# Performance work log

Hardware: AMD Instinct MI355X
Metric: run time of the kernel (lower is better)

The kernel has to match this reference:

```python
import jax, jax.numpy as jnp
import numpy as np

B, L1, L2 = 16, 32, 128
DEC = 512       # decoder_size
MEM = 512       # memory_bank_size
TOP = 50        # topic_num


def setup_inputs() -> dict:
    key = jax.random.key(0)
    ks = jax.random.split(key, 16)
    s = lambda fan_in: 1.0 / np.sqrt(fan_in)
    inp = {
        "decoder_state": jax.random.normal(ks[0], (B, DEC), jnp.float32),
        "doc_memory": jax.random.normal(ks[1], (B, L1, MEM), jnp.float32),
        "word_memory": jax.random.normal(ks[2], (B, L1, L2, MEM), jnp.float32),
        "topic_dist": jax.random.uniform(ks[3], (B, TOP), jnp.float32),
        "doc_mask": jnp.ones((B, L1), jnp.int32),
        "word_mask": jnp.ones((B, L1, L2), jnp.int32),
        # HierAttention params (PyTorch Linear weight layout: [out, in])
        "Wv": jax.random.uniform(ks[4], (1, DEC), jnp.float32, -s(DEC), s(DEC)),
        "Wd": jax.random.uniform(ks[5], (DEC, DEC), jnp.float32, -s(DEC), s(DEC)),
        "Wt": jax.random.uniform(ks[6], (DEC, TOP), jnp.float32, -s(TOP), s(TOP)),
        "Wm": jax.random.uniform(ks[7], (DEC, MEM), jnp.float32, -s(MEM), s(MEM)),
        # doc_attention (inner Attention) params
        "Wv2": jax.random.uniform(ks[8], (1, DEC), jnp.float32, -s(DEC), s(DEC)),
        "Wd2": jax.random.uniform(ks[9], (DEC, DEC), jnp.float32, -s(DEC), s(DEC)),
        "Wt2": jax.random.uniform(ks[10], (DEC, TOP), jnp.float32, -s(TOP), s(TOP)),
        "Wm2": jax.random.uniform(ks[11], (DEC, MEM), jnp.float32, -s(MEM), s(MEM)),
    }
    return inp


def reference(decoder_state, doc_memory, word_memory, topic_dist,
              doc_mask, word_mask,
              Wv, Wd, Wt, Wm, Wv2, Wd2, Wt2, Wm2):
    neg_inf = jnp.float32(-jnp.inf)

    # ---- word-level (HierAttention.score) ----
    enc_feat = jnp.einsum('bqwm,dm->bqwd', word_memory, Wm)      # [B,L1,L2,DEC]
    dec_feat = decoder_state @ Wd.T                              # [B,DEC]
    top_feat = topic_dist @ Wt.T                                 # [B,DEC]
    e = jnp.tanh(enc_feat + (dec_feat + top_feat)[:, None, None, :])
    word_scores = jnp.einsum('bqwd,od->bqw', e, Wv)[..., 0] if Wv.shape[0] != 1 else jnp.einsum('bqwd,d->bqw', e, Wv[0])
    word_scores = jnp.where(word_mask == 0, neg_inf, word_scores)
    word_attn = jax.nn.softmax(word_scores, axis=-1)             # [B,L1,L2]

    # ---- doc-level (Attention.score) ----
    enc_feat_d = jnp.einsum('bqm,dm->bqd', doc_memory, Wm2)      # [B,L1,DEC]
    dec_feat_d = decoder_state @ Wd2.T                           # [B,DEC]
    top_feat_d = topic_dist @ Wt2.T                              # [B,DEC]
    e_d = jnp.tanh(enc_feat_d + (dec_feat_d + top_feat_d)[:, None, :])
    doc_scores = jnp.einsum('bqd,d->bq', e_d, Wv2[0])            # [B,L1]
    doc_scores = jnp.where(doc_mask == 0, neg_inf, doc_scores)
    doc_attn = jax.nn.softmax(doc_scores, axis=-1)               # [B,L1]

    # ---- combine ----
    rescaled = doc_attn[..., None] * word_attn                   # [B,L1,L2]
    context = jnp.einsum('bqw,bqwm->bm', rescaled, word_memory)  # [B,MEM]
    return context, rescaled
```

## Files before the change

kernel.cpp:

```cpp
#include <hip/hip_runtime.h>
#include <hip/hip_bf16.h>
#include <math.h>

#define BATCH 16
#define L1 32
#define L2 128
#define DEC 512
#define MEM 512
#define TOPN 50
#define NROWS (BATCH * L1 * L2)
#define NBQ (BATCH * L1)

typedef short short8 __attribute__((ext_vector_type(8)));
typedef float f32x16 __attribute__((ext_vector_type(16)));

#define WS_WP     0
#define WS_WP2    131072
#define WS_BIAS1  262144
#define WS_BIAS2  270336
#define WS_DOCSC  278528

__device__ __forceinline__ unsigned int pkbf(float a, float b) {
    __hip_bfloat162 h = __float22bfloat162_rn(float2{a, b});
    union { __hip_bfloat162 h; unsigned int u; } c{h};
    return c.u;
}

__device__ __forceinline__ float fast_tanh(float x) {
    return 1.f - 2.f / (__expf(2.f * x) + 1.f);
}

__global__ __launch_bounds__(256) void setup_kernel(
    const float* __restrict__ Wm, const float* __restrict__ Wm2,
    unsigned short* __restrict__ Wp, unsigned short* __restrict__ Wp2,
    const float* __restrict__ dec, const float* __restrict__ topic,
    const float* __restrict__ Wd, const float* __restrict__ Wt,
    const float* __restrict__ Wd2, const float* __restrict__ Wt2,
    float* __restrict__ bias1, float* __restrict__ bias2,
    float* __restrict__ ctx_out)
{
    if (blockIdx.x < 128) {
        int s = blockIdx.x * 256 + threadIdx.x;
        int C = s >> 10;
        int u = s & 1023;
        int nt = u >> 6, k8 = (u >> 5) & 1, n_in = u & 31;
        int d = nt * 32 + n_in;
        int k = C * 16 + k8 * 8;

        const float* src = Wm + (size_t)d * DEC + k;
        uint4 v;
        v.x = pkbf(src[0], src[1]); v.y = pkbf(src[2], src[3]);
        v.z = pkbf(src[4], src[5]); v.w = pkbf(src[6], src[7]);
        ((uint4*)Wp)[s] = v;

        const float* src2 = Wm2 + (size_t)d * DEC + k;
        uint4 w;
        w.x = pkbf(src2[0], src2[1]); w.y = pkbf(src2[2], src2[3]);
        w.z = pkbf(src2[4], src2[5]); w.w = pkbf(src2[6], src2[7]);
        ((uint4*)Wp2)[s] = w;
    } else if (blockIdx.x < 160) {
        int idx = (blockIdx.x - 128) * 256 + threadIdx.x;
        int b = idx >> 9, d = idx & 511;
        float a1 = 0.f, a2 = 0.f;
        const float* db = dec + b * DEC;
        const float* w1 = Wd + (size_t)d * DEC;
        const float* w2 = Wd2 + (size_t)d * DEC;
#pragma unroll 4
        for (int k = 0; k < DEC; ++k) {
            float x = db[k];
            a1 = fmaf(x, w1[k], a1);
            a2 = fmaf(x, w2[k], a2);
        }
        const float* tb = topic + b * TOPN;
        const float* t1 = Wt + (size_t)d * TOPN;
        const float* t2 = Wt2 + (size_t)d * TOPN;
#pragma unroll 2
        for (int t = 0; t < TOPN; ++t) {
            float x = tb[t];
            a1 = fmaf(x, t1[t], a1);
            a2 = fmaf(x, t2[t], a2);
        }
        bias1[idx] = a1;
        bias2[idx] = a2;
    } else {
        int i = (blockIdx.x - 160) * 256 + threadIdx.x;
        float4 z = {0.f, 0.f, 0.f, 0.f};
        ((float4*)ctx_out)[i * 2] = z;
        ((float4*)ctx_out)[i * 2 + 1] = z;
    }
}

__global__ __launch_bounds__(256) void score_mfma_kernel(
    const float* __restrict__ X,
    const unsigned short* __restrict__ Wp,
    const float* __restrict__ Wv,
    const float* __restrict__ bias,
    float* __restrict__ scores,
    int bshift)
{
    __shared__ __align__(16) short lsA[256 * 8];
    __shared__ __align__(16) short lsB[2048 * 8];
    __shared__ float red[4][64];

    const int tid = threadIdx.x;
    const int lane = tid & 63;
    const int wid = tid >> 6;
    const int row0 = blockIdx.x * 64;

    const int srow = tid >> 2;
    const int kslot = tid & 3;
    const int sA = ((kslot >> 1) * 2 + (srow >> 5)) * 64 + (kslot & 1) * 32 + (srow & 31);
    const float4* xs4 = (const float4*)(X + (size_t)(row0 + srow) * DEC) + kslot * 2;

    const uint4* bsrc = (const uint4*)Wp + (size_t)wid * 512 + lane;

    f32x16 acc[8];
#pragma unroll
    for (int t = 0; t < 8; ++t)
        acc[t] = (f32x16){0.f,0.f,0.f,0.f, 0.f,0.f,0.f,0.f, 0.f,0.f,0.f,0.f, 0.f,0.f,0.f,0.f};

    const short8* lA = (const short8*)lsA;
    const short8* lB = (const short8*)lsB;

    for (int it = 0; it < 16; ++it) {
        uint4 bv[8];
#pragma unroll
        for (int i = 0; i < 8; ++i) bv[i] = bsrc[i * 64];
        bsrc += 2048;
#pragma unroll
        for (int i = 0; i < 8; ++i)
            *((uint4*)&lsB[((size_t)wid * 512 + i * 64 + lane) * 8]) = bv[i];

        float4 xv0 = xs4[0];
        float4 xv1 = xs4[1];
        xs4 += 8;
        union { unsigned int u[4]; short8 s; } xb;
        xb.u[0] = pkbf(xv0.x, xv0.y); xb.u[1] = pkbf(xv0.z, xv0.w);
        xb.u[2] = pkbf(xv1.x, xv1.y); xb.u[3] = pkbf(xv1.z, xv1.w);
        *((short8*)&lsA[sA * 8]) = xb.s;

        __syncthreads();

#pragma unroll
        for (int c = 0; c < 2; ++c) {
            short8 a0 = lA[(c * 2 + 0) * 64 + lane];
            short8 a1 = lA[(c * 2 + 1) * 64 + lane];
            short8 b0 = lB[c * 1024 + (wid * 4 + 0) * 64 + lane];
            short8 b1 = lB[c * 1024 + (wid * 4 + 1) * 64 + lane];
            short8 b2 = lB[c * 1024 + (wid * 4 + 2) * 64 + lane];
            short8 b3 = lB[c * 1024 + (wid * 4 + 3) * 64 + lane];
            acc[0] = __builtin_amdgcn_mfma_f32_32x32x16_bf16(a0, b0, acc[0], 0, 0, 0);
            acc[1] = __builtin_amdgcn_mfma_f32_32x32x16_bf16(a0, b1, acc[1], 0, 0, 0);
            acc[2] = __builtin_amdgcn_mfma_f32_32x32x16_bf16(a0, b2, acc[2], 0, 0, 0);
            acc[3] = __builtin_amdgcn_mfma_f32_32x32x16_bf16(a0, b3, acc[3], 0, 0, 0);
            acc[4] = __builtin_amdgcn_mfma_f32_32x32x16_bf16(a1, b0, acc[4], 0, 0, 0);
            acc[5] = __builtin_amdgcn_mfma_f32_32x32x16_bf16(a1, b1, acc[5], 0, 0, 0);
            acc[6] = __builtin_amdgcn_mfma_f32_32x32x16_bf16(a1, b2, acc[6], 0, 0, 0);
            acc[7] = __builtin_amdgcn_mfma_f32_32x32x16_bf16(a1, b3, acc[7], 0, 0, 0);
        }
        __syncthreads();
    }

    const int col = lane & 31;
    const int h = lane >> 5;
    float wv[4], bs[2][4];
    const int b0i = (row0) >> bshift;
    const int b1i = (row0 + 32) >> bshift;
#pragma unroll
    for (int nt = 0; nt < 4; ++nt) {
        int d = wid * 128 + nt * 32 + col;
        wv[nt] = Wv[d];
        bs[0][nt] = bias[b0i * DEC + d];
        bs[1][nt] = bias[b1i * DEC + d];
    }

#pragma unroll
    for (int mt = 0; mt < 2; ++mt) {
#pragma unroll
        for (int r = 0; r < 16; ++r) {
            float p = 0.f;
#pragma unroll
            for (int nt = 0; nt < 4; ++nt) {
                float x = acc[mt * 4 + nt][r] + bs[mt][nt];
                p = fmaf(wv[nt], fast_tanh(x), p);
            }
            p += __shfl_xor(p, 16);
            p += __shfl_xor(p, 8);
            p += __shfl_xor(p, 4);
            p += __shfl_xor(p, 2);
            p += __shfl_xor(p, 1);
            if (col == mt * 16 + r) {
                int row_in = (r & 3) + 8 * (r >> 2) + 4 * h;
                red[wid][mt * 32 + row_in] = p;
            }
        }
    }
    __syncthreads();
    if (tid < 64)
        scores[row0 + tid] = red[0][tid] + red[1][tid] + red[2][tid] + red[3][tid];
}

__global__ __launch_bounds__(512) void fused_word_kernel(
    const float* __restrict__ X,
    const unsigned short* __restrict__ Wp,
    const float* __restrict__ Wv,
    const float* __restrict__ bias1,
    const float* __restrict__ doc_scores,
    const int* __restrict__ doc_mask,
    const int* __restrict__ word_mask,
    float* __restrict__ rescaled_out,
    float* __restrict__ ctx_out)
{
    __shared__ __align__(16) short lsA[2 * 2048];
    __shared__ float red[8][128];
    __shared__ float sS[128];
    __shared__ float rmax2[2], rsum2[2];
    __shared__ float s_dattn;
    __shared__ __align__(16) float4 part[3 * 128];

    const int tid = threadIdx.x;
    const int lane = tid & 63;
    const int wid = tid >> 6;
    const int bq = blockIdx.x;
    const int r0 = bq * L2;
    const int b = bq >> 5;
    const int q = bq & 31;

    if (tid < 32) {
        int di = b * 32 + tid;
        float dsv = doc_scores[di];
        if (doc_mask[di] == 0) dsv = -INFINITY;
        float mx = dsv;
#pragma unroll
        for (int o = 1; o <= 16; o <<= 1) mx = fmaxf(mx, __shfl_xor(mx, o));
        float e = __expf(dsv - mx);
        float sum = e;
#pragma unroll
        for (int o = 1; o <= 16; o <<= 1) sum += __shfl_xor(sum, o);
        if (tid == q) s_dattn = e / sum;
    }

    const int row = tid >> 2;
    const int kq = tid & 3;
    const int mt_s = row >> 5;
    const int rl_s = row & 31;
    const int k8_s = kq >> 1;
    const int q4 = (kq & 1) * 4;
    const int slot_s = mt_s * 64 + k8_s * 32 + rl_s;
    const float4* xs = (const float4*)(X + (size_t)(r0 + row) * DEC) + kq;

    const uint4* Bp = (const uint4*)Wp;
    const int boff = wid * 128 + lane;

    f32x16 acc[8];
#pragma unroll
    for (int t = 0; t < 8; ++t)
        acc[t] = (f32x16){0.f,0.f,0.f,0.f, 0.f,0.f,0.f,0.f, 0.f,0.f,0.f,0.f, 0.f,0.f,0.f,0.f};

    const short8* lA = (const short8*)lsA;

    float4 va[4];
#pragma unroll
    for (int i = 0; i < 4; ++i) va[i] = xs[i * 4];
    uint4 ub0[2], ub1[2];
#pragma unroll
    for (int i = 0; i < 2; ++i) {
        ub0[i] = Bp[i * 1024 + boff];
        ub1[i] = Bp[i * 1024 + boff + 64];
    }

#pragma unroll
    for (int c = 0; c < 32; ++c) {
        const int p = c & 1;
        const int ia = c & 3;
        uint2 w2;
        w2.x = pkbf(va[ia].x, va[ia].y);
        w2.y = pkbf(va[ia].z, va[ia].w);
        *(uint2*)&lsA[(p * 256 + slot_s) * 8 + q4] = w2;
        __syncthreads();

        va[ia] = xs[((c + 4) & 31) * 4];
        uint4 nb0 = Bp[((c + 2) & 31) * 1024 + boff];
        uint4 nb1 = Bp[((c + 2) & 31) * 1024 + boff + 64];

        short8 a0 = lA[p * 256 + 0 * 64 + lane];
        short8 a1 = lA[p * 256 + 1 * 64 + lane];
        short8 a2 = lA[p * 256 + 2 * 64 + lane];
        short8 a3 = lA[p * 256 + 3 * 64 + lane];
        union { uint4 u; short8 s; } cb0{ub0[p]}, cb1{ub1[p]};
        acc[0] = __builtin_amdgcn_mfma_f32_32x32x16_bf16(a0, cb0.s, acc[0], 0, 0, 0);
        acc[1] = __builtin_amdgcn_mfma_f32_32x32x16_bf16(a0, cb1.s, acc[1], 0, 0, 0);
        acc[2] = __builtin_amdgcn_mfma_f32_32x32x16_bf16(a1, cb0.s, acc[2], 0, 0, 0);
        acc[3] = __builtin_amdgcn_mfma_f32_32x32x16_bf16(a1, cb1.s, acc[3], 0, 0, 0);
        acc[4] = __builtin_amdgcn_mfma_f32_32x32x16_bf16(a2, cb0.s, acc[4], 0, 0, 0);
        acc[5] = __builtin_amdgcn_mfma_f32_32x32x16_bf16(a2, cb1.s, acc[5], 0, 0, 0);
        acc[6] = __builtin_amdgcn_mfma_f32_32x32x16_bf16(a3, cb0.s, acc[6], 0, 0, 0);
        acc[7] = __builtin_amdgcn_mfma_f32_32x32x16_bf16(a3, cb1.s, acc[7], 0, 0, 0);

        ub0[p] = nb0; ub1[p] = nb1;
    }

    const int col = lane & 31;
    const int h = lane >> 5;
    float wv0, wv1, bs0, bs1;
    {
        int d0 = wid * 64 + col;
        int d1 = wid * 64 + 32 + col;
        wv0 = Wv[d0]; wv1 = Wv[d1];
        bs0 = bias1[b * DEC + d0]; bs1 = bias1[b * DEC + d1];
    }
#pragma unroll
    for (int mt = 0; mt < 4; ++mt) {
#pragma unroll
        for (int r = 0; r < 16; ++r) {
            float p = fmaf(wv0, fast_tanh(acc[mt * 2 + 0][r] + bs0),
                           wv1 * fast_tanh(acc[mt * 2 + 1][r] + bs1));
            p += __shfl_xor(p, 16);
            p += __shfl_xor(p, 8);
            p += __shfl_xor(p, 4);
            p += __shfl_xor(p, 2);
            p += __shfl_xor(p, 1);
            if (col == r) {
                int row_in = (r & 3) + 8 * (r >> 2) + 4 * h;
                red[wid][mt * 32 + row_in] = p;
            }
        }
    }
    __syncthreads();

    float e = 0.f, sv = 0.f;
    if (tid < 128) {
        sv = red[0][tid] + red[1][tid] + red[2][tid] + red[3][tid]
           + red[4][tid] + red[5][tid] + red[6][tid] + red[7][tid];
        if (word_mask[r0 + tid] == 0) sv = -INFINITY;
        float mx = sv;
#pragma unroll
        for (int o = 1; o <= 32; o <<= 1) mx = fmaxf(mx, __shfl_xor(mx, o));
        if (lane == 0) rmax2[wid] = mx;
    }
    __syncthreads();
    if (tid < 128) {
        float mx = fmaxf(rmax2[0], rmax2[1]);
        e = __expf(sv - mx);
        float sum = e;
#pragma unroll
        for (int o = 1; o <= 32; o <<= 1) sum += __shfl_xor(sum, o);
        if (lane == 0) rsum2[wid] = sum;
    }
    __syncthreads();
    if (tid < 128) {
        float sum = rsum2[0] + rsum2[1];
        float resc = s_dattn * (e / sum);
        sS[tid] = resc;
        rescaled_out[r0 + tid] = resc;
    }
    __syncthreads();

    const int hh = tid >> 7;
    const int m4 = tid & 127;
    const float4* Xr = (const float4*)X + (size_t)r0 * 128 + (size_t)hh * 32 * 128 + m4;
    float4 a = {0.f, 0.f, 0.f, 0.f};
#pragma unroll 8
    for (int i = 0; i < 32; ++i) {
        float rr = sS[hh * 32 + i];
        float4 v = Xr[(size_t)i * 128];
        a.x = fmaf(rr, v.x, a.x);
        a.y = fmaf(rr, v.y, a.y);
        a.z = fmaf(rr, v.z, a.z);
        a.w = fmaf(rr, v.w, a.w);
    }
    if (hh) part[(hh - 1) * 128 + m4] = a;
    __syncthreads();
    if (hh == 0) {
        float4 p0 = part[m4], p1 = part[128 + m4], p2 = part[256 + m4];
        a.x += p0.x + p1.x + p2.x;
        a.y += p0.y + p1.y + p2.y;
        a.z += p0.z + p1.z + p2.z;
        a.w += p0.w + p1.w + p2.w;
        float* dst = ctx_out + (size_t)b * MEM + m4 * 4;
        atomicAdd(dst + 0, a.x);
        atomicAdd(dst + 1, a.y);
        atomicAdd(dst + 2, a.z);
        atomicAdd(dst + 3, a.w);
    }
}

extern "C" void kernel_launch(void* const* d_in, const int* in_sizes, int n_in,
                              void* d_out, int out_size, void* d_ws, size_t ws_size,
                              hipStream_t stream) {
    const float* decoder_state = (const float*)d_in[0];
    const float* doc_memory    = (const float*)d_in[1];
    const float* word_memory   = (const float*)d_in[2];
    const float* topic_dist    = (const float*)d_in[3];
    const int*   doc_mask      = (const int*)d_in[4];
    const int*   word_mask     = (const int*)d_in[5];
    const float* Wv  = (const float*)d_in[6];
    const float* Wd  = (const float*)d_in[7];
    const float* Wt  = (const float*)d_in[8];
    const float* Wm  = (const float*)d_in[9];
    const float* Wv2 = (const float*)d_in[10];
    const float* Wd2 = (const float*)d_in[11];
    const float* Wt2 = (const float*)d_in[12];
    const float* Wm2 = (const float*)d_in[13];

    float* ws = (float*)d_ws;
    unsigned short* Wp  = (unsigned short*)(ws + WS_WP);
    unsigned short* Wp2 = (unsigned short*)(ws + WS_WP2);
    float* bias1       = ws + WS_BIAS1;
    float* bias2       = ws + WS_BIAS2;
    float* doc_scores  = ws + WS_DOCSC;

    float* ctx_out      = (float*)d_out;
    float* rescaled_out = (float*)d_out + BATCH * MEM;

    setup_kernel<<<164, 256, 0, stream>>>(Wm, Wm2, Wp, Wp2,
                                          decoder_state, topic_dist,
                                          Wd, Wt, Wd2, Wt2, bias1, bias2, ctx_out);
    score_mfma_kernel<<<NBQ / 64, 256, 0, stream>>>(doc_memory, Wp2, Wv2, bias2, doc_scores, 5);
    fused_word_kernel<<<NBQ, 512, 0, stream>>>(word_memory, Wp, Wv, bias1,
                                               doc_scores, doc_mask, word_mask,
                                               rescaled_out, ctx_out);
}
```

Baseline: 350.3 us.

## Process two K-chunks per barrier with four LDS buffers and MFMA priority

Restructures the main GEMM loop of the fused word kernel so that each iteration stages two K-chunks of the activation tile into a four-slot LDS ring. Only one barrier is issued per pair of chunks, which halves the number of workgroup barriers. The barrier is now a raw s_barrier preceded by an explicit lgkmcnt wait. The MFMA sequences are wrapped in s_setprio to favour matrix issue across waves. This raises LDS usage and register pressure from the extra weight prefetch buffers, which could lower occupancy.

```diff
diff --git a/kernel.cpp b/kernel.cpp
--- a/kernel.cpp
+++ b/kernel.cpp
@@ -211,7 +211,7 @@
     float* __restrict__ rescaled_out,
     float* __restrict__ ctx_out)
 {
-    __shared__ __align__(16) short lsA[2 * 2048];
+    __shared__ __align__(16) short lsA[4 * 2048];
     __shared__ float red[8][128];
     __shared__ float sS[128];
     __shared__ float rmax2[2], rsum2[2];
@@ -262,42 +262,73 @@
     float4 va[4];
 #pragma unroll
     for (int i = 0; i < 4; ++i) va[i] = xs[i * 4];
-    uint4 ub0[2], ub1[2];
-#pragma unroll
-    for (int i = 0; i < 2; ++i) {
-        ub0[i] = Bp[i * 1024 + boff];
-        ub1[i] = Bp[i * 1024 + boff + 64];
-    }
-
-#pragma unroll
-    for (int c = 0; c < 32; ++c) {
-        const int p = c & 1;
-        const int ia = c & 3;
-        uint2 w2;
-        w2.x = pkbf(va[ia].x, va[ia].y);
-        w2.y = pkbf(va[ia].z, va[ia].w);
-        *(uint2*)&lsA[(p * 256 + slot_s) * 8 + q4] = w2;
-        __syncthreads();
-
-        va[ia] = xs[((c + 4) & 31) * 4];
-        uint4 nb0 = Bp[((c + 2) & 31) * 1024 + boff];
-        uint4 nb1 = Bp[((c + 2) & 31) * 1024 + boff + 64];
-
-        short8 a0 = lA[p * 256 + 0 * 64 + lane];
-        short8 a1 = lA[p * 256 + 1 * 64 + lane];
-        short8 a2 = lA[p * 256 + 2 * 64 + lane];
-        short8 a3 = lA[p * 256 + 3 * 64 + lane];
-        union { uint4 u; short8 s; } cb0{ub0[p]}, cb1{ub1[p]};
-        acc[0] = __builtin_amdgcn_mfma_f32_32x32x16_bf16(a0, cb0.s, acc[0], 0, 0, 0);
-        acc[1] = __builtin_amdgcn_mfma_f32_32x32x16_bf16(a0, cb1.s, acc[1], 0, 0, 0);
-        acc[2] = __builtin_amdgcn_mfma_f32_32x32x16_bf16(a1, cb0.s, acc[2], 0, 0, 0);
-        acc[3] = __builtin_amdgcn_mfma_f32_32x32x16_bf16(a1, cb1.s, acc[3], 0, 0, 0);
-        acc[4] = __builtin_amdgcn_mfma_f32_32x32x16_bf16(a2, cb0.s, acc[4], 0, 0, 0);
-        acc[5] = __builtin_amdgcn_mfma_f32_32x32x16_bf16(a2, cb1.s, acc[5], 0, 0, 0);
-        acc[6] = __builtin_amdgcn_mfma_f32_32x32x16_bf16(a3, cb0.s, acc[6], 0, 0, 0);
-        acc[7] = __builtin_amdgcn_mfma_f32_32x32x16_bf16(a3, cb1.s, acc[7], 0, 0, 0);
-
-        ub0[p] = nb0; ub1[p] = nb1;
+    uint4 ubb[2][2][2];
+#pragma unroll
+    for (int j = 0; j < 2; ++j) {
+        ubb[0][j][0] = Bp[j * 1024 + boff];
+        ubb[0][j][1] = Bp[j * 1024 + boff + 64];
+    }
+
+#pragma unroll
+    for (int cc = 0; cc < 16; ++cc) {
+        const int c0 = cc * 2, c1 = cc * 2 + 1;
+        const int b0 = c0 & 3, b1 = c1 & 3;
+        const int s = cc & 1;
+
+        {
+            uint2 w0, w1;
+            w0.x = pkbf(va[b0].x, va[b0].y);
+            w0.y = pkbf(va[b0].z, va[b0].w);
+            w1.x = pkbf(va[b1].x, va[b1].y);
+            w1.y = pkbf(va[b1].z, va[b1].w);
+            *(uint2*)&lsA[(b0 * 256 + slot_s) * 8 + q4] = w0;
+            *(uint2*)&lsA[(b1 * 256 + slot_s) * 8 + q4] = w1;
+        }
+        asm volatile("s_waitcnt lgkmcnt(0)" ::: "memory");
+        __builtin_amdgcn_s_barrier();
+        asm volatile("" ::: "memory");
+
+        va[b0] = xs[((c0 + 4) & 31) * 4];
+        va[b1] = xs[((c1 + 4) & 31) * 4];
+        ubb[s ^ 1][0][0] = Bp[((c0 + 2) & 31) * 1024 + boff];
+        ubb[s ^ 1][0][1] = Bp[((c0 + 2) & 31) * 1024 + boff + 64];
+        ubb[s ^ 1][1][0] = Bp[((c1 + 2) & 31) * 1024 + boff];
+        ubb[s ^ 1][1][1] = Bp[((c1 + 2) & 31) * 1024 + boff + 64];
+
+        {
+            short8 a0 = lA[b0 * 256 + 0 * 64 + lane];
+            short8 a1 = lA[b0 * 256 + 1 * 64 + lane];
+            short8 a2 = lA[b0 * 256 + 2 * 64 + lane];
+            short8 a3 = lA[b0 * 256 + 3 * 64 + lane];
+            union { uint4 u; short8 s8; } cb0{ubb[s][0][0]}, cb1{ubb[s][0][1]};
+            __builtin_amdgcn_s_setprio(1);
+            acc[0] = __builtin_amdgcn_mfma_f32_32x32x16_bf16(a0, cb0.s8, acc[0], 0, 0, 0);
+            acc[1] = __builtin_amdgcn_mfma_f32_32x32x16_bf16(a0, cb1.s8, acc[1], 0, 0, 0);
+            acc[2] = __builtin_amdgcn_mfma_f32_32x32x16_bf16(a1, cb0.s8, acc[2], 0, 0, 0);
+            acc[3] = __builtin_amdgcn_mfma_f32_32x32x16_bf16(a1, cb1.s8, acc[3], 0, 0, 0);
+            acc[4] = __builtin_amdgcn_mfma_f32_32x32x16_bf16(a2, cb0.s8, acc[4], 0, 0, 0);
+            acc[5] = __builtin_amdgcn_mfma_f32_32x32x16_bf16(a2, cb1.s8, acc[5], 0, 0, 0);
+            acc[6] = __builtin_amdgcn_mfma_f32_32x32x16_bf16(a3, cb0.s8, acc[6], 0, 0, 0);
+            acc[7] = __builtin_amdgcn_mfma_f32_32x32x16_bf16(a3, cb1.s8, acc[7], 0, 0, 0);
+            __builtin_amdgcn_s_setprio(0);
+        }
+        {
+            short8 a0 = lA[b1 * 256 + 0 * 64 + lane];
+            short8 a1 = lA[b1 * 256 + 1 * 64 + lane];
+            short8 a2 = lA[b1 * 256 + 2 * 64 + lane];
+            short8 a3 = lA[b1 * 256 + 3 * 64 + lane];
+            union { uint4 u; short8 s8; } cb0{ubb[s][1][0]}, cb1{ubb[s][1][1]};
+            __builtin_amdgcn_s_setprio(1);
+            acc[0] = __builtin_amdgcn_mfma_f32_32x32x16_bf16(a0, cb0.s8, acc[0], 0, 0, 0);
+            acc[1] = __builtin_amdgcn_mfma_f32_32x32x16_bf16(a0, cb1.s8, acc[1], 0, 0, 0);
+            acc[2] = __builtin_amdgcn_mfma_f32_32x32x16_bf16(a1, cb0.s8, acc[2], 0, 0, 0);
+            acc[3] = __builtin_amdgcn_mfma_f32_32x32x16_bf16(a1, cb1.s8, acc[3], 0, 0, 0);
+            acc[4] = __builtin_amdgcn_mfma_f32_32x32x16_bf16(a2, cb0.s8, acc[4], 0, 0, 0);
+            acc[5] = __builtin_amdgcn_mfma_f32_32x32x16_bf16(a2, cb1.s8, acc[5], 0, 0, 0);
+            acc[6] = __builtin_amdgcn_mfma_f32_32x32x16_bf16(a3, cb0.s8, acc[6], 0, 0, 0);
+            acc[7] = __builtin_amdgcn_mfma_f32_32x32x16_bf16(a3, cb1.s8, acc[7], 0, 0, 0);
+            __builtin_amdgcn_s_setprio(0);
+        }
     }
 
     const int col = lane & 31;
```

New measurement: 352.4 us. Within noise of the previous version (+0.6%).

## Stage full bf16 A tile in LDS once and split N into two passes

Applied to the files above, without the earlier changes.

The fused word kernel used to convert X to bf16 in small double-buffered LDS chunks with a barrier on every k-step. It now converts the whole 128x512 A tile into a padded LDS buffer using four barriers. The 8 waves are split 2 (rows) x 4 (columns), and the 512 output columns are covered in two passes of 256 with 4 accumulators each, running the tanh/Wv epilogue after each pass. The goal is to cut per-step barriers and accumulator register pressure, at the cost of about 132KB of LDS per block, which limits occupancy to one block per CU.

```diff
diff --git a/kernel.cpp b/kernel.cpp
--- a/kernel.cpp
+++ b/kernel.cpp
@@ -211,7 +211,7 @@
     float* __restrict__ rescaled_out,
     float* __restrict__ ctx_out)
 {
-    __shared__ __align__(16) short lsA[2 * 2048];
+    __shared__ __align__(16) char lsA[64 * 2064];
     __shared__ float red[8][128];
     __shared__ float sS[128];
     __shared__ float rmax2[2], rsum2[2];
@@ -221,10 +221,74 @@
     const int tid = threadIdx.x;
     const int lane = tid & 63;
     const int wid = tid >> 6;
+    const int wr = wid & 1;
+    const int wd = wid >> 1;
     const int bq = blockIdx.x;
     const int r0 = bq * L2;
     const int b = bq >> 5;
     const int q = bq & 31;
+    const int col = lane & 31;
+    const int h = lane >> 5;
+
+    const float4* Xs = (const float4*)X + (size_t)(r0 + (tid >> 5)) * 128 + (tid & 31);
+    char* const wbase = lsA + (((tid & 31) >> 1) * 2064) + ((tid >> 5) << 4) + ((tid & 1) << 3);
+
+#define ISSUE(dst, ks) { _Pragma("unroll") \
+    for (int i = 0; i < 8; ++i) dst[i] = Xs[(size_t)(i * 16) * 128 + (ks) * 32]; }
+
+#define WRITEA(src, ks) { char* wp = wbase + (ks) * 16 * 2064; _Pragma("unroll") \
+    for (int i = 0; i < 8; ++i) { uint2 w; \
+        w.x = pkbf(src[i].x, src[i].y); w.y = pkbf(src[i].z, src[i].w); \
+        *(uint2*)(wp + i * 256) = w; } }
+
+#define LGKMBAR { asm volatile("s_waitcnt lgkmcnt(0)" ::: "memory"); \
+                  __builtin_amdgcn_s_barrier(); asm volatile("" ::: "memory"); }
+
+    const uint4* Bp = (const uint4*)Wp;
+    const size_t bB = (size_t)wd * 128 + lane;
+#define BOFFC(t, nt) ((size_t)(((t) & 31)) * 1024 + ((((t) >> 5) & 1)) * 512 + bB + (nt) * 64)
+
+    const char* const aP = lsA + (lane >> 5) * 2064 + ((wr * 64) + (lane & 31)) * 16;
+#define MFMA(a, bb, c) __builtin_amdgcn_mfma_f32_32x32x16_bf16(a, bb, c, 0, 0, 0)
+
+    f32x16 acc[4];
+#pragma unroll
+    for (int t = 0; t < 4; ++t)
+        acc[t] = (f32x16){0.f,0.f,0.f,0.f, 0.f,0.f,0.f,0.f, 0.f,0.f,0.f,0.f, 0.f,0.f,0.f,0.f};
+
+    uint4 ub[2][2];
+
+#define CHUNK(t) { \
+    union { uint4 u; short8 s8; } c0{ub[(t) & 1][0]}, c1{ub[(t) & 1][1]}; \
+    ub[(t) & 1][0] = Bp[BOFFC(((t) + 2) & 63, 0)]; \
+    ub[(t) & 1][1] = Bp[BOFFC(((t) + 2) & 63, 1)]; \
+    short8 a0 = *(const short8*)(aP + ((t) & 31) * 4128); \
+    short8 a1 = *(const short8*)(aP + ((t) & 31) * 4128 + 512); \
+    acc[0] = MFMA(a0, c0.s8, acc[0]); \
+    acc[1] = MFMA(a0, c1.s8, acc[1]); \
+    acc[2] = MFMA(a1, c0.s8, acc[2]); \
+    acc[3] = MFMA(a1, c1.s8, acc[3]); }
+
+#define CHUNK8(base) { CHUNK((base)+0) CHUNK((base)+1) CHUNK((base)+2) CHUNK((base)+3) \
+                       CHUNK((base)+4) CHUNK((base)+5) CHUNK((base)+6) CHUNK((base)+7) }
+
+#define EPILOGUE(p) { \
+    int d0 = (p) * 256 + wd * 64 + col; \
+    float wv0 = Wv[d0], wv1 = Wv[d0 + 32]; \
+    float bs0 = bias1[b * DEC + d0], bs1 = bias1[b * DEC + d0 + 32]; \
+    _Pragma("unroll") for (int mt = 0; mt < 2; ++mt) { \
+      _Pragma("unroll") for (int r = 0; r < 16; ++r) { \
+        float val = fmaf(wv0, fast_tanh(acc[mt * 2 + 0][r] + bs0), \
+                         wv1 * fast_tanh(acc[mt * 2 + 1][r] + bs1)); \
+        val += __shfl_xor(val, 16); val += __shfl_xor(val, 8); \
+        val += __shfl_xor(val, 4);  val += __shfl_xor(val, 2); \
+        val += __shfl_xor(val, 1); \
+        if (col == r) red[(p) * 4 + wd][wr * 64 + mt * 32 + ((r & 3) + 8 * (r >> 2) + 4 * h)] = val; \
+      } } }
+
+    float4 vA[8], vB[8];
+    ISSUE(vA, 0);
+    ISSUE(vB, 1);
 
     if (tid < 32) {
         int di = b * 32 + tid;
@@ -240,92 +304,64 @@
         if (tid == q) s_dattn = e / sum;
     }
 
-    const int row = tid >> 2;
-    const int kq = tid & 3;
-    const int mt_s = row >> 5;
-    const int rl_s = row & 31;
-    const int k8_s = kq >> 1;
-    const int q4 = (kq & 1) * 4;
-    const int slot_s = mt_s * 64 + k8_s * 32 + rl_s;
-    const float4* xs = (const float4*)(X + (size_t)(r0 + row) * DEC) + kq;
-
-    const uint4* Bp = (const uint4*)Wp;
-    const int boff = wid * 128 + lane;
-
-    f32x16 acc[8];
-#pragma unroll
-    for (int t = 0; t < 8; ++t)
+    WRITEA(vA, 0);
+    ub[0][0] = Bp[BOFFC(0, 0)];
+    ub[0][1] = Bp[BOFFC(0, 1)];
+    ub[1][0] = Bp[BOFFC(1, 0)];
+    ub[1][1] = Bp[BOFFC(1, 1)];
+    LGKMBAR;
+    ISSUE(vA, 2);
+    CHUNK8(0);
+    WRITEA(vB, 1);
+    LGKMBAR;
+    ISSUE(vB, 3);
+    CHUNK8(8);
+    WRITEA(vA, 2);
+    LGKMBAR;
+    CHUNK8(16);
+    WRITEA(vB, 3);
+    LGKMBAR;
+    CHUNK8(24);
+
+    EPILOGUE(0);
+
+#pragma unroll
+    for (int t = 0; t < 4; ++t)
         acc[t] = (f32x16){0.f,0.f,0.f,0.f, 0.f,0.f,0.f,0.f, 0.f,0.f,0.f,0.f, 0.f,0.f,0.f,0.f};
 
-    const short8* lA = (const short8*)lsA;
-
-    float4 va[4];
-#pragma unroll
-    for (int i = 0; i < 4; ++i) va[i] = xs[i * 4];
-    uint4 ub0[2], ub1[2];
-#pragma unroll
-    for (int i = 0; i < 2; ++i) {
-        ub0[i] = Bp[i * 1024 + boff];
-        ub1[i] = Bp[i * 1024 + boff + 64];
-    }
-
-#pragma unroll
-    for (int c = 0; c < 32; ++c) {
-        const int p = c & 1;
-        const int ia = c & 3;
-        uint2 w2;
-        w2.x = pkbf(va[ia].x, va[ia].y);
-        w2.y = pkbf(va[ia].z, va[ia].w);
-        *(uint2*)&lsA[(p * 256 + slot_s) * 8 + q4] = w2;
-        __syncthreads();
-
-        va[ia] = xs[((c + 4) & 31) * 4];
-        uint4 nb0 = Bp[((c + 2) & 31) * 1024 + boff];
-        uint4 nb1 = Bp[((c + 2) & 31) * 1024 + boff + 64];
-
-        short8 a0 = lA[p * 256 + 0 * 64 + lane];
-        short8 a1 = lA[p * 256 + 1 * 64 + lane];
-        short8 a2 = lA[p * 256 + 2 * 64 + lane];
-        short8 a3 = lA[p * 256 + 3 * 64 + lane];
-        union { uint4 u; short8 s; } cb0{ub0[p]}, cb1{ub1[p]};
-        acc[0] = __builtin_amdgcn_mfma_f32_32x32x16_bf16(a0, cb0.s, acc[0], 0, 0, 0);
-        acc[1] = __builtin_amdgcn_mfma_f32_32x32x16_bf16(a0, cb1.s, acc[1], 0, 0, 0);
-        acc[2] = __builtin_amdgcn_mfma_f32_32x32x16_bf16(a1, cb0.s, acc[2], 0, 0, 0);
-        acc[3] = __builtin_amdgcn_mfma_f32_32x32x16_bf16(a1, cb1.s, acc[3], 0, 0, 0);
-        acc[4] = __builtin_amdgcn_mfma_f32_32x32x16_bf16(a2, cb0.s, acc[4], 0, 0, 0);
-        acc[5] = __builtin_amdgcn_mfma_f32_32x32x16_bf16(a2, cb1.s, acc[5], 0, 0, 0);
-        acc[6] = __builtin_amdgcn_mfma_f32_32x32x16_bf16(a3, cb0.s, acc[6], 0, 0, 0);
-        acc[7] = __builtin_amdgcn_mfma_f32_32x32x16_bf16(a3, cb1.s, acc[7], 0, 0, 0);
-
-        ub0[p] = nb0; ub1[p] = nb1;
-    }
-
-    const int col = lane & 31;
-    const int h = lane >> 5;
-    float wv0, wv1, bs0, bs1;
-    {
-        int d0 = wid * 64 + col;
-        int d1 = wid * 64 + 32 + col;
-        wv0 = Wv[d0]; wv1 = Wv[d1];
-        bs0 = bias1[b * DEC + d0]; bs1 = bias1[b * DEC + d1];
-    }
-#pragma unroll
-    for (int mt = 0; mt < 4; ++mt) {
-#pragma unroll
-        for (int r = 0; r < 16; ++r) {
-            float p = fmaf(wv0, fast_tanh(acc[mt * 2 + 0][r] + bs0),
-                           wv1 * fast_tanh(acc[mt * 2 + 1][r] + bs1));
-            p += __shfl_xor(p, 16);
-            p += __shfl_xor(p, 8);
-            p += __shfl_xor(p, 4);
-            p += __shfl_xor(p, 2);
-            p += __shfl_xor(p, 1);
-            if (col == r) {
-                int row_in = (r & 3) + 8 * (r >> 2) + 4 * h;
-                red[wid][mt * 32 + row_in] = p;
-            }
-        }
-    }
+#pragma unroll 2
+    for (int j = 0; j < 16; ++j) {
+        const int c0 = 2 * j, c1 = 2 * j + 1;
+        {
+            union { uint4 u; short8 s8; } d00{ub[0][0]}, d01{ub[0][1]};
+            int tt = (32 + c0 + 2) & 63;
+            size_t off = (size_t)(tt & 31) * 1024 + ((tt >> 5) & 1) * 512 + bB;
+            ub[0][0] = Bp[off];
+            ub[0][1] = Bp[off + 64];
+            short8 a0 = *(const short8*)(aP + c0 * 4128);
+            short8 a1 = *(const short8*)(aP + c0 * 4128 + 512);
+            acc[0] = MFMA(a0, d00.s8, acc[0]);
+            acc[1] = MFMA(a0, d01.s8, acc[1]);
+            acc[2] = MFMA(a1, d00.s8, acc[2]);
+            acc[3] = MFMA(a1, d01.s8, acc[3]);
+        }
+        {
+            union { uint4 u; short8 s8; } d10{ub[1][0]}, d11{ub[1][1]};
+            int tt = (32 + c1 + 2) & 63;
+            size_t off = (size_t)(tt & 31) * 1024 + ((tt >> 5) & 1) * 512 + bB;
+            ub[1][0] = Bp[off];
+            ub[1][1] = Bp[off + 64];
+            short8 a0 = *(const short8*)(aP + c1 * 4128);
+            short8 a1 = *(const short8*)(aP + c1 * 4128 + 512);
+            acc[0] = MFMA(a0, d10.s8, acc[0]);
+            acc[1] = MFMA(a0, d11.s8, acc[1]);
+            acc[2] = MFMA(a1, d10.s8, acc[2]);
+            acc[3] = MFMA(a1, d11.s8, acc[3]);
+        }
+    }
+
+    EPILOGUE(1);
+
     __syncthreads();
 
     float e = 0.f, sv = 0.f;
```

After: 367.4 us. +4.9%, slower.

## Split word scoring from combine, merge doc/word score GEMMs, warp-parallel bias GEMV

Applied to the files above, without the earlier changes.

Pulls the word-score MFMA GEMM out of the fused per-(b,q) kernel into one score kernel that also handles the doc scores. That kernel stages a full 64x512 bf16 A tile in padded LDS once and streams B fragments from global memory through registers. A separate combine kernel then reads the raw scores back from the rescaled output buffer, applies softmax and accumulates the context. The bias GEMVs are rewritten to give one wave per output element, with vectorized loads and a shuffle reduction, replacing the serial per-thread loop. The cost is that word_memory is now read twice from global memory, and raw scores make an extra round trip through the output buffer.

```diff
diff --git a/kernel.cpp b/kernel.cpp
--- a/kernel.cpp
+++ b/kernel.cpp
@@ -39,184 +39,210 @@
     float* __restrict__ bias1, float* __restrict__ bias2,
     float* __restrict__ ctx_out)
 {
-    if (blockIdx.x < 128) {
-        int s = blockIdx.x * 256 + threadIdx.x;
+    const int bid = blockIdx.x;
+    const int tid = threadIdx.x;
+    if (bid < 128) {
+        int s = bid * 256 + tid;
         int C = s >> 10;
         int u = s & 1023;
         int nt = u >> 6, k8 = (u >> 5) & 1, n_in = u & 31;
         int d = nt * 32 + n_in;
         int k = C * 16 + k8 * 8;
 
-        const float* src = Wm + (size_t)d * DEC + k;
+        const float4* src = (const float4*)(Wm + (size_t)d * DEC + k);
+        float4 v0 = src[0], v1 = src[1];
         uint4 v;
-        v.x = pkbf(src[0], src[1]); v.y = pkbf(src[2], src[3]);
-        v.z = pkbf(src[4], src[5]); v.w = pkbf(src[6], src[7]);
+        v.x = pkbf(v0.x, v0.y); v.y = pkbf(v0.z, v0.w);
+        v.z = pkbf(v1.x, v1.y); v.w = pkbf(v1.z, v1.w);
         ((uint4*)Wp)[s] = v;
 
-        const float* src2 = Wm2 + (size_t)d * DEC + k;
+        const float4* src2 = (const float4*)(Wm2 + (size_t)d * DEC + k);
+        float4 w0 = src2[0], w1 = src2[1];
         uint4 w;
-        w.x = pkbf(src2[0], src2[1]); w.y = pkbf(src2[2], src2[3]);
-        w.z = pkbf(src2[4], src2[5]); w.w = pkbf(src2[6], src2[7]);
+        w.x = pkbf(w0.x, w0.y); w.y = pkbf(w0.z, w0.w);
+        w.z = pkbf(w1.x, w1.y); w.w = pkbf(w1.z, w1.w);
         ((uint4*)Wp2)[s] = w;
-    } else if (blockIdx.x < 160) {
-        int idx = (blockIdx.x - 128) * 256 + threadIdx.x;
-        int b = idx >> 9, d = idx & 511;
-        float a1 = 0.f, a2 = 0.f;
-        const float* db = dec + b * DEC;
-        const float* w1 = Wd + (size_t)d * DEC;
-        const float* w2 = Wd2 + (size_t)d * DEC;
-#pragma unroll 4
-        for (int k = 0; k < DEC; ++k) {
-            float x = db[k];
-            a1 = fmaf(x, w1[k], a1);
-            a2 = fmaf(x, w2[k], a2);
-        }
-        const float* tb = topic + b * TOPN;
-        const float* t1 = Wt + (size_t)d * TOPN;
-        const float* t2 = Wt2 + (size_t)d * TOPN;
-#pragma unroll 2
-        for (int t = 0; t < TOPN; ++t) {
-            float x = tb[t];
-            a1 = fmaf(x, t1[t], a1);
-            a2 = fmaf(x, t2[t], a2);
-        }
-        bias1[idx] = a1;
-        bias2[idx] = a2;
+    } else if (bid < 128 + 4096) {
+        int gw = (bid - 128) * 4 + (tid >> 6);
+        int lane = tid & 63;
+        int mat = gw >> 13;
+        int rem = gw & 8191;
+        int bb = rem >> 9;
+        int d = rem & 511;
+
+        const float* wrow = (mat ? Wd2 : Wd) + (size_t)d * DEC;
+        const float* drow = dec + (size_t)bb * DEC;
+        float4 a0 = ((const float4*)wrow)[lane * 2];
+        float4 a1 = ((const float4*)wrow)[lane * 2 + 1];
+        float4 x0 = ((const float4*)drow)[lane * 2];
+        float4 x1 = ((const float4*)drow)[lane * 2 + 1];
+        float acc = a0.x * x0.x;
+        acc = fmaf(a0.y, x0.y, acc);
+        acc = fmaf(a0.z, x0.z, acc);
+        acc = fmaf(a0.w, x0.w, acc);
+        acc = fmaf(a1.x, x1.x, acc);
+        acc = fmaf(a1.y, x1.y, acc);
+        acc = fmaf(a1.z, x1.z, acc);
+        acc = fmaf(a1.w, x1.w, acc);
+        const float* trow = (mat ? Wt2 : Wt) + (size_t)d * TOPN;
+        if (lane < TOPN) acc = fmaf(trow[lane], topic[bb * TOPN + lane], acc);
+#pragma unroll
+        for (int o = 1; o <= 32; o <<= 1) acc += __shfl_xor(acc, o);
+        if (lane == 0) (mat ? bias2 : bias1)[bb * DEC + d] = acc;
     } else {
-        int i = (blockIdx.x - 160) * 256 + threadIdx.x;
+        int i = (bid - (128 + 4096)) * 256 + tid;
         float4 z = {0.f, 0.f, 0.f, 0.f};
         ((float4*)ctx_out)[i * 2] = z;
         ((float4*)ctx_out)[i * 2 + 1] = z;
     }
 }
 
-__global__ __launch_bounds__(256) void score_mfma_kernel(
-    const float* __restrict__ X,
+__global__ __launch_bounds__(256, 2) void score_all_kernel(
+    const float* __restrict__ Xw,
+    const float* __restrict__ Xd,
     const unsigned short* __restrict__ Wp,
-    const float* __restrict__ Wv,
-    const float* __restrict__ bias,
-    float* __restrict__ scores,
-    int bshift)
+    const unsigned short* __restrict__ Wp2,
+    const float* __restrict__ Wv, const float* __restrict__ Wv2,
+    const float* __restrict__ bias1, const float* __restrict__ bias2,
+    float* __restrict__ word_scores,
+    float* __restrict__ doc_scores)
 {
-    __shared__ __align__(16) short lsA[256 * 8];
-    __shared__ __align__(16) short lsB[2048 * 8];
+    __shared__ __align__(16) char lsA[64 * 1040];
     __shared__ float red[4][64];
 
+    const int bid = blockIdx.x;
     const int tid = threadIdx.x;
+    const bool isdoc = (bid >= 1024);
+
+    const float* X;
+    const unsigned short* Wpp;
+    const float* Wvp;
+    const float* bias;
+    float* outp;
+    int r0, bshift;
+    if (isdoc) { X = Xd; Wpp = Wp2; Wvp = Wv2; bias = bias2; outp = doc_scores; r0 = (bid - 1024) * 64; bshift = 5; }
+    else       { X = Xw; Wpp = Wp;  Wvp = Wv;  bias = bias1; outp = word_scores; r0 = bid * 64; bshift = 12; }
+
+    {
+        const int kf4 = tid & 127;
+        const int rb0 = tid >> 7;
+        const float4* Xs = (const float4*)X + (size_t)r0 * 128 + kf4;
+        float4 va[8], vb[8];
+#pragma unroll
+        for (int i = 0; i < 8; ++i) va[i] = Xs[(size_t)(2 * i + rb0) * 128];
+#pragma unroll
+        for (int blk = 0; blk < 4; ++blk) {
+            float4* cur = (blk & 1) ? vb : va;
+            float4* nxt = (blk & 1) ? va : vb;
+            if (blk < 3) {
+#pragma unroll
+                for (int i = 0; i < 8; ++i)
+                    nxt[i] = Xs[(size_t)(2 * (8 * (blk + 1) + i) + rb0) * 128];
+            }
+#pragma unroll
+            for (int i = 0; i < 8; ++i) {
+                int row = 2 * (8 * blk + i) + rb0;
+                uint2 w;
+                w.x = pkbf(cur[i].x, cur[i].y);
+                w.y = pkbf(cur[i].z, cur[i].w);
+                *(uint2*)(lsA + (size_t)row * 1040 + kf4 * 8) = w;
+            }
+        }
+    }
+    __syncthreads();
+
     const int lane = tid & 63;
     const int wid = tid >> 6;
-    const int row0 = blockIdx.x * 64;
-
-    const int srow = tid >> 2;
-    const int kslot = tid & 3;
-    const int sA = ((kslot >> 1) * 2 + (srow >> 5)) * 64 + (kslot & 1) * 32 + (srow & 31);
-    const float4* xs4 = (const float4*)(X + (size_t)(row0 + srow) * DEC) + kslot * 2;
-
-    const uint4* bsrc = (const uint4*)Wp + (size_t)wid * 512 + lane;
-
-    f32x16 acc[8];
-#pragma unroll
-    for (int t = 0; t < 8; ++t)
-        acc[t] = (f32x16){0.f,0.f,0.f,0.f, 0.f,0.f,0.f,0.f, 0.f,0.f,0.f,0.f, 0.f,0.f,0.f,0.f};
-
-    const short8* lA = (const short8*)lsA;
-    const short8* lB = (const short8*)lsB;
-
-    for (int it = 0; it < 16; ++it) {
-        uint4 bv[8];
-#pragma unroll
-        for (int i = 0; i < 8; ++i) bv[i] = bsrc[i * 64];
-        bsrc += 2048;
-#pragma unroll
-        for (int i = 0; i < 8; ++i)
-            *((uint4*)&lsB[((size_t)wid * 512 + i * 64 + lane) * 8]) = bv[i];
-
-        float4 xv0 = xs4[0];
-        float4 xv1 = xs4[1];
-        xs4 += 8;
-        union { unsigned int u[4]; short8 s; } xb;
-        xb.u[0] = pkbf(xv0.x, xv0.y); xb.u[1] = pkbf(xv0.z, xv0.w);
-        xb.u[2] = pkbf(xv1.x, xv1.y); xb.u[3] = pkbf(xv1.z, xv1.w);
-        *((short8*)&lsA[sA * 8]) = xb.s;
-
-        __syncthreads();
-
-#pragma unroll
-        for (int c = 0; c < 2; ++c) {
-            short8 a0 = lA[(c * 2 + 0) * 64 + lane];
-            short8 a1 = lA[(c * 2 + 1) * 64 + lane];
-            short8 b0 = lB[c * 1024 + (wid * 4 + 0) * 64 + lane];
-            short8 b1 = lB[c * 1024 + (wid * 4 + 1) * 64 + lane];
-            short8 b2 = lB[c * 1024 + (wid * 4 + 2) * 64 + lane];
-            short8 b3 = lB[c * 1024 + (wid * 4 + 3) * 64 + lane];
-            acc[0] = __builtin_amdgcn_mfma_f32_32x32x16_bf16(a0, b0, acc[0], 0, 0, 0);
-            acc[1] = __builtin_amdgcn_mfma_f32_32x32x16_bf16(a0, b1, acc[1], 0, 0, 0);
-            acc[2] = __builtin_amdgcn_mfma_f32_32x32x16_bf16(a0, b2, acc[2], 0, 0, 0);
-            acc[3] = __builtin_amdgcn_mfma_f32_32x32x16_bf16(a0, b3, acc[3], 0, 0, 0);
-            acc[4] = __builtin_amdgcn_mfma_f32_32x32x16_bf16(a1, b0, acc[4], 0, 0, 0);
-            acc[5] = __builtin_amdgcn_mfma_f32_32x32x16_bf16(a1, b1, acc[5], 0, 0, 0);
-            acc[6] = __builtin_amdgcn_mfma_f32_32x32x16_bf16(a1, b2, acc[6], 0, 0, 0);
-            acc[7] = __builtin_amdgcn_mfma_f32_32x32x16_bf16(a1, b3, acc[7], 0, 0, 0);
-        }
-        __syncthreads();
-    }
-
     const int col = lane & 31;
     const int h = lane >> 5;
-    float wv[4], bs[2][4];
-    const int b0i = (row0) >> bshift;
-    const int b1i = (row0 + 32) >> bshift;
-#pragma unroll
-    for (int nt = 0; nt < 4; ++nt) {
-        int d = wid * 128 + nt * 32 + col;
-        wv[nt] = Wv[d];
-        bs[0][nt] = bias[b0i * DEC + d];
-        bs[1][nt] = bias[b1i * DEC + d];
-    }
-
-#pragma unroll
-    for (int mt = 0; mt < 2; ++mt) {
-#pragma unroll
-        for (int r = 0; r < 16; ++r) {
-            float p = 0.f;
-#pragma unroll
-            for (int nt = 0; nt < 4; ++nt) {
-                float x = acc[mt * 4 + nt][r] + bs[mt][nt];
-                p = fmaf(wv[nt], fast_tanh(x), p);
-            }
-            p += __shfl_xor(p, 16);
-            p += __shfl_xor(p, 8);
-            p += __shfl_xor(p, 4);
-            p += __shfl_xor(p, 2);
-            p += __shfl_xor(p, 1);
-            if (col == mt * 16 + r) {
-                int row_in = (r & 3) + 8 * (r >> 2) + 4 * h;
-                red[wid][mt * 32 + row_in] = p;
+
+    const char* aB0 = lsA + (size_t)col * 1040 + h * 16;
+    const char* aB1 = aB0 + 32 * 1040;
+
+    const uint4* Bq = (const uint4*)Wpp;
+    const int bBase = wid * 128 + lane;
+#define BOFF(s) ((size_t)((s) & 31) * 1024 + (size_t)((s) >> 5) * 512 + bBase)
+#define MFMA(a, bb, c) __builtin_amdgcn_mfma_f32_32x32x16_bf16(a, bb, c, 0, 0, 0)
+
+    uint4 rbf[8][2];
+#pragma unroll
+    for (int i = 0; i < 8; ++i) { rbf[i][0] = Bq[BOFF(i)]; rbf[i][1] = Bq[BOFF(i) + 64]; }
+
+    float preg0 = 0.f, preg1 = 0.f;
+    const int b0i = (r0) >> bshift;
+    const int b1i = (r0 + 32) >> bshift;
+
+#pragma unroll
+    for (int P = 0; P < 2; ++P) {
+        f32x16 acc0, acc1, acc2, acc3;
+        acc0 = acc1 = acc2 = acc3 =
+            (f32x16){0.f,0.f,0.f,0.f, 0.f,0.f,0.f,0.f, 0.f,0.f,0.f,0.f, 0.f,0.f,0.f,0.f};
+#pragma unroll
+        for (int t = 0; t < 32; ++t) {
+            const int s = P * 32 + t;
+            short8 a0 = *(const short8*)(aB0 + t * 32);
+            short8 a1 = *(const short8*)(aB1 + t * 32);
+            union { uint4 u; short8 s8; } c0{rbf[s & 7][0]}, c1{rbf[s & 7][1]};
+            if (s < 56) { rbf[s & 7][0] = Bq[BOFF(s + 8)]; rbf[s & 7][1] = Bq[BOFF(s + 8) + 64]; }
+            acc0 = MFMA(a0, c0.s8, acc0);
+            acc1 = MFMA(a0, c1.s8, acc1);
+            acc2 = MFMA(a1, c0.s8, acc2);
+            acc3 = MFMA(a1, c1.s8, acc3);
+        }
+        const int d0 = P * 256 + wid * 64 + col;
+        const float wv0 = Wvp[d0], wv1 = Wvp[d0 + 32];
+        {
+            const float bs0 = bias[b0i * DEC + d0], bs1 = bias[b0i * DEC + d0 + 32];
+#pragma unroll
+            for (int r = 0; r < 16; ++r) {
+                float val = fmaf(wv0, fast_tanh(acc0[r] + bs0),
+                                 wv1 * fast_tanh(acc1[r] + bs1));
+                val += __shfl_xor(val, 16);
+                val += __shfl_xor(val, 8);
+                val += __shfl_xor(val, 4);
+                val += __shfl_xor(val, 2);
+                val += __shfl_xor(val, 1);
+                preg0 += (col == r) ? val : 0.f;
             }
         }
+        {
+            const float bs0 = bias[b1i * DEC + d0], bs1 = bias[b1i * DEC + d0 + 32];
+#pragma unroll
+            for (int r = 0; r < 16; ++r) {
+                float val = fmaf(wv0, fast_tanh(acc2[r] + bs0),
+                                 wv1 * fast_tanh(acc3[r] + bs1));
+                val += __shfl_xor(val, 16);
+                val += __shfl_xor(val, 8);
+                val += __shfl_xor(val, 4);
+                val += __shfl_xor(val, 2);
+                val += __shfl_xor(val, 1);
+                preg1 += (col == r) ? val : 0.f;
+            }
+        }
+    }
+
+    const int rowin = (col & 3) + 8 * (col >> 2) + 4 * h;
+    if (col < 16) {
+        red[wid][rowin] = preg0;
+        red[wid][32 + rowin] = preg1;
     }
     __syncthreads();
     if (tid < 64)
-        scores[row0 + tid] = red[0][tid] + red[1][tid] + red[2][tid] + red[3][tid];
-}
-
-__global__ __launch_bounds__(512) void fused_word_kernel(
+        outp[r0 + tid] = red[0][tid] + red[1][tid] + red[2][tid] + red[3][tid];
+}
+
+__global__ __launch_bounds__(256, 4) void combine_kernel(
     const float* __restrict__ X,
-    const unsigned short* __restrict__ Wp,
-    const float* __restrict__ Wv,
-    const float* __restrict__ bias1,
     const float* __restrict__ doc_scores,
     const int* __restrict__ doc_mask,
     const int* __restrict__ word_mask,
     float* __restrict__ rescaled_out,
     float* __restrict__ ctx_out)
 {
-    __shared__ __align__(16) short lsA[2 * 2048];
-    __shared__ float red[8][128];
     __shared__ float sS[128];
     __shared__ float rmax2[2], rsum2[2];
     __shared__ float s_dattn;
-    __shared__ __align__(16) float4 part[3 * 128];
+    __shared__ __align__(16) float4 part[128];
 
     const int tid = threadIdx.x;
     const int lane = tid & 63;
@@ -240,98 +266,9 @@
         if (tid == q) s_dattn = e / sum;
     }
 
-    const int row = tid >> 2;
-    const int kq = tid & 3;
-    const int mt_s = row >> 5;
-    const int rl_s = row & 31;
-    const int k8_s = kq >> 1;
-    const int q4 = (kq & 1) * 4;
-    const int slot_s = mt_s * 64 + k8_s * 32 + rl_s;
-    const float4* xs = (const float4*)(X + (size_t)(r0 + row) * DEC) + kq;
-
-    const uint4* Bp = (const uint4*)Wp;
-    const int boff = wid * 128 + lane;
-
-    f32x16 acc[8];
-#pragma unroll
-    for (int t = 0; t < 8; ++t)
-        acc[t] = (f32x16){0.f,0.f,0.f,0.f, 0.f,0.f,0.f,0.f, 0.f,0.f,0.f,0.f, 0.f,0.f,0.f,0.f};
-
-    const short8* lA = (const short8*)lsA;
-
-    float4 va[4];
-#pragma unroll
-    for (int i = 0; i < 4; ++i) va[i] = xs[i * 4];
-    uint4 ub0[2], ub1[2];
-#pragma unroll
-    for (int i = 0; i < 2; ++i) {
-        ub0[i] = Bp[i * 1024 + boff];
-        ub1[i] = Bp[i * 1024 + boff + 64];
-    }
-
-#pragma unroll
-    for (int c = 0; c < 32; ++c) {
-        const int p = c & 1;
-        const int ia = c & 3;
-        uint2 w2;
-        w2.x = pkbf(va[ia].x, va[ia].y);
-        w2.y = pkbf(va[ia].z, va[ia].w);
-        *(uint2*)&lsA[(p * 256 + slot_s) * 8 + q4] = w2;
-        __syncthreads();
-
-        va[ia] = xs[((c + 4) & 31) * 4];
-        uint4 nb0 = Bp[((c + 2) & 31) * 1024 + boff];
-        uint4 nb1 = Bp[((c + 2) & 31) * 1024 + boff + 64];
-
-        short8 a0 = lA[p * 256 + 0 * 64 + lane];
-        short8 a1 = lA[p * 256 + 1 * 64 + lane];
-        short8 a2 = lA[p * 256 + 2 * 64 + lane];
-        short8 a3 = lA[p * 256 + 3 * 64 + lane];
-        union { uint4 u; short8 s; } cb0{ub0[p]}, cb1{ub1[p]};
-        acc[0] = __builtin_amdgcn_mfma_f32_32x32x16_bf16(a0, cb0.s, acc[0], 0, 0, 0);
-        acc[1] = __builtin_amdgcn_mfma_f32_32x32x16_bf16(a0, cb1.s, acc[1], 0, 0, 0);
-        acc[2] = __builtin_amdgcn_mfma_f32_32x32x16_bf16(a1, cb0.s, acc[2], 0, 0, 0);
-        acc[3] = __builtin_amdgcn_mfma_f32_32x32x16_bf16(a1, cb1.s, acc[3], 0, 0, 0);
-        acc[4] = __builtin_amdgcn_mfma_f32_32x32x16_bf16(a2, cb0.s, acc[4], 0, 0, 0);
-        acc[5] = __builtin_amdgcn_mfma_f32_32x32x16_bf16(a2, cb1.s, acc[5], 0, 0, 0);
-        acc[6] = __builtin_amdgcn_mfma_f32_32x32x16_bf16(a3, cb0.s, acc[6], 0, 0, 0);
-        acc[7] = __builtin_amdgcn_mfma_f32_32x32x16_bf16(a3, cb1.s, acc[7], 0, 0, 0);
-
-        ub0[p] = nb0; ub1[p] = nb1;
-    }
-
-    const int col = lane & 31;
-    const int h = lane >> 5;
-    float wv0, wv1, bs0, bs1;
-    {
-        int d0 = wid * 64 + col;
-        int d1 = wid * 64 + 32 + col;
-        wv0 = Wv[d0]; wv1 = Wv[d1];
-        bs0 = bias1[b * DEC + d0]; bs1 = bias1[b * DEC + d1];
-    }
-#pragma unroll
-    for (int mt = 0; mt < 4; ++mt) {
-#pragma unroll
-        for (int r = 0; r < 16; ++r) {
-            float p = fmaf(wv0, fast_tanh(acc[mt * 2 + 0][r] + bs0),
-                           wv1 * fast_tanh(acc[mt * 2 + 1][r] + bs1));
-            p += __shfl_xor(p, 16);
-            p += __shfl_xor(p, 8);
-            p += __shfl_xor(p, 4);
-            p += __shfl_xor(p, 2);
-            p += __shfl_xor(p, 1);
-            if (col == r) {
-                int row_in = (r & 3) + 8 * (r >> 2) + 4 * h;
-                red[wid][mt * 32 + row_in] = p;
-            }
-        }
-    }
-    __syncthreads();
-
     float e = 0.f, sv = 0.f;
     if (tid < 128) {
-        sv = red[0][tid] + red[1][tid] + red[2][tid] + red[3][tid]
-           + red[4][tid] + red[5][tid] + red[6][tid] + red[7][tid];
+        sv = rescaled_out[r0 + tid];
         if (word_mask[r0 + tid] == 0) sv = -INFINITY;
         float mx = sv;
 #pragma unroll
@@ -358,25 +295,22 @@
 
     const int hh = tid >> 7;
     const int m4 = tid & 127;
-    const float4* Xr = (const float4*)X + (size_t)r0 * 128 + (size_t)hh * 32 * 128 + m4;
+    const float4* Xr = (const float4*)X + (size_t)(r0 + hh * 64) * 128 + m4;
     float4 a = {0.f, 0.f, 0.f, 0.f};
 #pragma unroll 8
-    for (int i = 0; i < 32; ++i) {
-        float rr = sS[hh * 32 + i];
+    for (int i = 0; i < 64; ++i) {
+        float rr = sS[hh * 64 + i];
         float4 v = Xr[(size_t)i * 128];
         a.x = fmaf(rr, v.x, a.x);
         a.y = fmaf(rr, v.y, a.y);
         a.z = fmaf(rr, v.z, a.z);
         a.w = fmaf(rr, v.w, a.w);
     }
-    if (hh) part[(hh - 1) * 128 + m4] = a;
+    if (hh) part[m4] = a;
     __syncthreads();
     if (hh == 0) {
-        float4 p0 = part[m4], p1 = part[128 + m4], p2 = part[256 + m4];
-        a.x += p0.x + p1.x + p2.x;
-        a.y += p0.y + p1.y + p2.y;
-        a.z += p0.z + p1.z + p2.z;
-        a.w += p0.w + p1.w + p2.w;
+        float4 p0 = part[m4];
+        a.x += p0.x; a.y += p0.y; a.z += p0.z; a.w += p0.w;
         float* dst = ctx_out + (size_t)b * MEM + m4 * 4;
         atomicAdd(dst + 0, a.x);
         atomicAdd(dst + 1, a.y);
@@ -413,11 +347,12 @@
     float* ctx_out      = (float*)d_out;
     float* rescaled_out = (float*)d_out + BATCH * MEM;
 
-    setup_kernel<<<164, 256, 0, stream>>>(Wm, Wm2, Wp, Wp2,
-                                          decoder_state, topic_dist,
-                                          Wd, Wt, Wd2, Wt2, bias1, bias2, ctx_out);
-    score_mfma_kernel<<<NBQ / 64, 256, 0, stream>>>(doc_memory, Wp2, Wv2, bias2, doc_scores, 5);
-    fused_word_kernel<<<NBQ, 512, 0, stream>>>(word_memory, Wp, Wv, bias1,
-                                               doc_scores, doc_mask, word_mask,
-                                               rescaled_out, ctx_out);
-}
+    setup_kernel<<<128 + 4096 + 4, 256, 0, stream>>>(Wm, Wm2, Wp, Wp2,
+                                                     decoder_state, topic_dist,
+                                                     Wd, Wt, Wd2, Wt2, bias1, bias2, ctx_out);
+    score_all_kernel<<<1024 + 8, 256, 0, stream>>>(word_memory, doc_memory, Wp, Wp2,
+                                                   Wv, Wv2, bias1, bias2,
+                                                   rescaled_out, doc_scores);
+    combine_kernel<<<NBQ, 256, 0, stream>>>(word_memory, doc_scores, doc_mask, word_mask,
+                                            rescaled_out, ctx_out);
+}
```

Result: faster. 342.0 us (-2.4%).
